# Kernel tuning notes

Measured on AMD Instinct MI355X. Metric: run time of the kernel, lower is better.

Reference implementation:

```python
import jax, jax.numpy as jnp
import numpy as np

HIDDEN = 2048
INTER = 1408
NUM_EXPERTS = 8
TOP_K = 2
BATCH, SEQ = 2, 1024


def setup_inputs() -> dict:
    key = jax.random.key(0)
    ks = jax.random.split(key, 8)
    s = 0.02
    return {
        "x": jax.random.normal(ks[0], (BATCH, SEQ, HIDDEN), dtype=jnp.float32),
        "router_w": jax.random.normal(ks[1], (NUM_EXPERTS, HIDDEN), dtype=jnp.float32) * s,
        "gate_w": jax.random.normal(ks[2], (NUM_EXPERTS, INTER, HIDDEN), dtype=jnp.float32) * s,
        "up_w": jax.random.normal(ks[3], (NUM_EXPERTS, INTER, HIDDEN), dtype=jnp.float32) * s,
        "down_w": jax.random.normal(ks[4], (NUM_EXPERTS, HIDDEN, INTER), dtype=jnp.float32) * s,
        "shared_gate_w": jax.random.normal(ks[5], (INTER, HIDDEN), dtype=jnp.float32) * s,
        "shared_up_w": jax.random.normal(ks[6], (INTER, HIDDEN), dtype=jnp.float32) * s,
        "shared_down_w": jax.random.normal(ks[7], (HIDDEN, INTER), dtype=jnp.float32) * s,
    }


def reference(x, router_w, gate_w, up_w, down_w,
              shared_gate_w, shared_up_w, shared_down_w):
    B, S, H = x.shape
    T = B * S
    E = router_w.shape[0]
    xf = x.reshape(T, H)

    # Router: softmax over experts, top-k selection, renormalized weights
    logits = xf @ router_w.T                       # [T, E]
    probs = jax.nn.softmax(logits, axis=-1)
    topw, topi = jax.lax.top_k(probs, TOP_K)       # [T, K]
    topw = topw / jnp.sum(topw, axis=-1, keepdims=True)

    # Combine weight per (token, expert): scatter-add of top-k weights
    comb = jnp.zeros((T, E), dtype=xf.dtype).at[
        jnp.arange(T)[:, None], topi].add(topw)    # [T, E]

    # All-expert SwiGLU (grouped GEMM form of masked gather/MLP/scatter)
    g = jnp.einsum('th,eih->tei', xf, gate_w)      # [T, E, I]
    u = jnp.einsum('th,eih->tei', xf, up_w)
    hmid = jax.nn.silu(g) * u
    eo = jnp.einsum('tei,ehi->teh', hmid, down_w)  # [T, E, H]
    out = jnp.einsum('te,teh->th', comb, eo)       # weighted combine

    # Shared expert applied to every token
    sh = (jax.nn.silu(xf @ shared_gate_w.T) * (xf @ shared_up_w.T)) @ shared_down_w.T
    out = out + sh
    return out.reshape(B, S, H)
```

## Files before the change

### kernel.cpp

```cpp
#include <hip/hip_runtime.h>
#include <cstdint>
#include <cstddef>

#define T_TOK 2048
#define HID   2048
#define INTER 1408
#define NEXP  8
#define NPAIR 6144
#define LDST  40

typedef __bf16 bf16x8 __attribute__((ext_vector_type(8)));
typedef float  floatx4 __attribute__((ext_vector_type(4)));

static const size_t XB_OFF   = 0;
static const size_t HM_OFF   = XB_OFF + (size_t)T_TOK * HID * 2;
static const size_t TOK_OFF  = HM_OFF + (size_t)NPAIR * INTER * 2;
static const size_t WGT_OFF  = TOK_OFF + (size_t)NPAIR * 4;
static const size_t TE_OFF   = WGT_OFF + (size_t)NPAIR * 4;
static const size_t TW_OFF   = TE_OFF + (size_t)T_TOK * 2 * 4;
static const size_t CTRL_OFF = TW_OFF + (size_t)T_TOK * 2 * 4;

static __device__ __forceinline__ unsigned short f2bf(float f) {
    unsigned u = __float_as_uint(f);
    u += 0x7fffu + ((u >> 16) & 1u);
    return (unsigned short)(u >> 16);
}
static __device__ __forceinline__ unsigned pk2(float a, float b) {
    return (unsigned)f2bf(a) | ((unsigned)f2bf(b) << 16);
}

__global__ __launch_bounds__(256) void k_cvt_x(const float* __restrict__ x,
                                               unsigned short* __restrict__ xb) {
    int gid = blockIdx.x * 256 + threadIdx.x;
    const float4* src = (const float4*)x;
    float4 a = src[gid * 2], b = src[gid * 2 + 1];
    uint4 o;
    o.x = pk2(a.x, a.y); o.y = pk2(a.z, a.w);
    o.z = pk2(b.x, b.y); o.w = pk2(b.z, b.w);
    ((uint4*)xb)[gid] = o;
}

__global__ __launch_bounds__(256) void k_router(const float* __restrict__ x,
                                                const float* __restrict__ rw,
                                                int* __restrict__ te, float* __restrict__ tw,
                                                int* __restrict__ counts) {
    int wave = threadIdx.x >> 6, lane = threadIdx.x & 63;
    int t = blockIdx.x * 4 + wave;
    const float* xp = x + (size_t)t * HID;

    float acc[8];
#pragma unroll
    for (int e = 0; e < 8; ++e) acc[e] = 0.f;
    for (int i = lane; i < HID; i += 64) {
        float xv = xp[i];
#pragma unroll
        for (int e = 0; e < 8; ++e) acc[e] = fmaf(xv, rw[e * HID + i], acc[e]);
    }
#pragma unroll
    for (int e = 0; e < 8; ++e) {
        float v = acc[e];
        for (int s = 32; s; s >>= 1) v += __shfl_xor(v, s, 64);
        acc[e] = v;
    }
    float mx = acc[0];
#pragma unroll
    for (int e = 1; e < 8; ++e) mx = fmaxf(mx, acc[e]);
    float p[8];
#pragma unroll
    for (int e = 0; e < 8; ++e) p[e] = __expf(acc[e] - mx);
    int i1 = 0; float v1 = p[0];
#pragma unroll
    for (int e = 1; e < 8; ++e) if (p[e] > v1) { v1 = p[e]; i1 = e; }
    int i2 = -1; float v2 = -1.f;
#pragma unroll
    for (int e = 0; e < 8; ++e) if (e != i1 && p[e] > v2) { v2 = p[e]; i2 = e; }
    float inv = 1.f / (v1 + v2);
    if (lane == 0) {
        te[2 * t] = i1;     tw[2 * t] = v1 * inv;
        te[2 * t + 1] = i2; tw[2 * t + 1] = v2 * inv;
        atomicAdd(&counts[i1], 1);
        atomicAdd(&counts[i2], 1);
    }
}

__global__ void k_offsets(int* __restrict__ ctrl) {
    if (threadIdx.x == 0) {
        int s = 0;
        for (int e = 0; e < 8; ++e) { ctrl[16 + e] = s; s += ctrl[e]; }
        ctrl[16 + 8] = s;
        ctrl[8] = T_TOK;
    }
}

__global__ __launch_bounds__(256) void k_scatter(const int* __restrict__ te,
                                                 const float* __restrict__ tw,
                                                 const int* __restrict__ offsets,
                                                 int* __restrict__ fill,
                                                 int* __restrict__ tok, float* __restrict__ wgt) {
    int t = blockIdx.x * 256 + threadIdx.x;
    if (t >= T_TOK) return;
#pragma unroll
    for (int k = 0; k < 2; ++k) {
        int e = te[2 * t + k];
        int slot = atomicAdd(&fill[e], 1);
        int pp = offsets[e] + slot;
        tok[pp] = t; wgt[pp] = tw[2 * t + k];
    }
    tok[2 * T_TOK + t] = t; wgt[2 * T_TOK + t] = 1.0f;
}

__global__ __launch_bounds__(256) void k_gemm1(const unsigned short* __restrict__ xb,
                                               const float* __restrict__ gate_w,
                                               const float* __restrict__ up_w,
                                               const float* __restrict__ sgate,
                                               const float* __restrict__ sup,
                                               const int* __restrict__ tok,
                                               const int* __restrict__ ctrl,
                                               unsigned short* __restrict__ hmid) {
    int e = blockIdx.z;
    int cnt = ctrl[e];
    int m0 = blockIdx.y * 128;
    if (m0 >= cnt) return;
    int off = ctrl[16 + e];
    int i0 = blockIdx.x * 64;
    const float* gw = (e < 8) ? gate_w + (size_t)e * INTER * HID : sgate;
    const float* uw = (e < 8) ? up_w + (size_t)e * INTER * HID : sup;

    __shared__ __align__(16) unsigned short As[128 * LDST];
    __shared__ __align__(16) unsigned short Bg[64 * LDST];
    __shared__ __align__(16) unsigned short Bu[64 * LDST];

    int tid = threadIdx.x;
    int lane = tid & 63, wave = tid >> 6;
    int ar = tid >> 1, ac = (tid & 1) * 16;
    int ap = off + m0 + ar; if (ap > NPAIR - 1) ap = NPAIR - 1;
    const unsigned short* asrc = xb + (size_t)tok[ap] * HID + ac;
    int br = tid >> 2, bc = (tid & 3) * 8;
    const float* gsrc = gw + (size_t)(i0 + br) * HID + bc;
    const float* usrc = uw + (size_t)(i0 + br) * HID + bc;

    floatx4 accg[2][4], accu[2][4];
#pragma unroll
    for (int mi = 0; mi < 2; ++mi)
#pragma unroll
        for (int ni = 0; ni < 4; ++ni) {
            accg[mi][ni] = (floatx4){0.f, 0.f, 0.f, 0.f};
            accu[mi][ni] = (floatx4){0.f, 0.f, 0.f, 0.f};
        }

    int wm = wave * 32;
    int mrow = lane & 15, kq = (lane >> 4) * 8;

    for (int kt = 0; kt < HID / 32; ++kt) {
        int h0 = kt * 32;
        uint4 av0 = *(const uint4*)(asrc + h0);
        uint4 av1 = *(const uint4*)(asrc + h0 + 8);
        float4 g0 = *(const float4*)(gsrc + h0);
        float4 g1 = *(const float4*)(gsrc + h0 + 4);
        float4 u0 = *(const float4*)(usrc + h0);
        float4 u1 = *(const float4*)(usrc + h0 + 4);
        __syncthreads();
        *(uint4*)&As[ar * LDST + ac] = av0;
        *(uint4*)&As[ar * LDST + ac + 8] = av1;
        uint4 bg; bg.x = pk2(g0.x, g0.y); bg.y = pk2(g0.z, g0.w);
        bg.z = pk2(g1.x, g1.y); bg.w = pk2(g1.z, g1.w);
        *(uint4*)&Bg[br * LDST + bc] = bg;
        uint4 bu; bu.x = pk2(u0.x, u0.y); bu.y = pk2(u0.z, u0.w);
        bu.z = pk2(u1.x, u1.y); bu.w = pk2(u1.z, u1.w);
        *(uint4*)&Bu[br * LDST + bc] = bu;
        __syncthreads();

        bf16x8 af[2];
#pragma unroll
        for (int mi = 0; mi < 2; ++mi)
            af[mi] = *(const bf16x8*)&As[(wm + mi * 16 + mrow) * LDST + kq];
#pragma unroll
        for (int ni = 0; ni < 4; ++ni) {
            bf16x8 bgv = *(const bf16x8*)&Bg[(ni * 16 + mrow) * LDST + kq];
            bf16x8 buv = *(const bf16x8*)&Bu[(ni * 16 + mrow) * LDST + kq];
#pragma unroll
            for (int mi = 0; mi < 2; ++mi) {
                accg[mi][ni] = __builtin_amdgcn_mfma_f32_16x16x32_bf16(af[mi], bgv, accg[mi][ni], 0, 0, 0);
                accu[mi][ni] = __builtin_amdgcn_mfma_f32_16x16x32_bf16(af[mi], buv, accu[mi][ni], 0, 0, 0);
            }
        }
    }

    int quad = lane >> 4, col = lane & 15;
#pragma unroll
    for (int mi = 0; mi < 2; ++mi)
#pragma unroll
        for (int ni = 0; ni < 4; ++ni)
#pragma unroll
            for (int r = 0; r < 4; ++r) {
                int row = m0 + wm + mi * 16 + quad * 4 + r;
                if (row < cnt) {
                    float g = accg[mi][ni][r], u = accu[mi][ni][r];
                    float s = g / (1.f + __expf(-g));
                    hmid[(size_t)(off + row) * INTER + i0 + ni * 16 + col] = f2bf(s * u);
                }
            }
}

__global__ __launch_bounds__(256) void k_gemm2(const unsigned short* __restrict__ hmid,
                                               const float* __restrict__ down_w,
                                               const float* __restrict__ sdown,
                                               const int* __restrict__ tok,
                                               const float* __restrict__ wgt,
                                               const int* __restrict__ ctrl,
                                               float* __restrict__ out) {
    int e = blockIdx.z;
    int cnt = ctrl[e];
    int m0 = blockIdx.y * 128;
    if (m0 >= cnt) return;
    int off = ctrl[16 + e];
    int n0 = blockIdx.x * 64;
    const float* dw = (e < 8) ? down_w + (size_t)e * HID * INTER : sdown;

    __shared__ __align__(16) unsigned short As[128 * LDST];
    __shared__ __align__(16) unsigned short Bd[64 * LDST];

    int tid = threadIdx.x;
    int lane = tid & 63, wave = tid >> 6;
    int ar = tid >> 1, ac = (tid & 1) * 16;
    int ap = off + m0 + ar; if (ap > NPAIR - 1) ap = NPAIR - 1;
    const unsigned short* asrc = hmid + (size_t)ap * INTER + ac;
    int br = tid >> 2, bc = (tid & 3) * 8;
    const float* bsrc = dw + (size_t)(n0 + br) * INTER + bc;

    floatx4 acc[2][4];
#pragma unroll
    for (int mi = 0; mi < 2; ++mi)
#pragma unroll
        for (int ni = 0; ni < 4; ++ni) acc[mi][ni] = (floatx4){0.f, 0.f, 0.f, 0.f};

    int wm = wave * 32;
    int mrow = lane & 15, kq = (lane >> 4) * 8;

    for (int kt = 0; kt < INTER / 32; ++kt) {
        int k0 = kt * 32;
        uint4 av0 = *(const uint4*)(asrc + k0);
        uint4 av1 = *(const uint4*)(asrc + k0 + 8);
        float4 b0 = *(const float4*)(bsrc + k0);
        float4 b1 = *(const float4*)(bsrc + k0 + 4);
        __syncthreads();
        *(uint4*)&As[ar * LDST + ac] = av0;
        *(uint4*)&As[ar * LDST + ac + 8] = av1;
        uint4 bd; bd.x = pk2(b0.x, b0.y); bd.y = pk2(b0.z, b0.w);
        bd.z = pk2(b1.x, b1.y); bd.w = pk2(b1.z, b1.w);
        *(uint4*)&Bd[br * LDST + bc] = bd;
        __syncthreads();

        bf16x8 af[2];
#pragma unroll
        for (int mi = 0; mi < 2; ++mi)
            af[mi] = *(const bf16x8*)&As[(wm + mi * 16 + mrow) * LDST + kq];
#pragma unroll
        for (int ni = 0; ni < 4; ++ni) {
            bf16x8 bv = *(const bf16x8*)&Bd[(ni * 16 + mrow) * LDST + kq];
#pragma unroll
            for (int mi = 0; mi < 2; ++mi)
                acc[mi][ni] = __builtin_amdgcn_mfma_f32_16x16x32_bf16(af[mi], bv, acc[mi][ni], 0, 0, 0);
        }
    }

    int quad = lane >> 4, col = lane & 15;
#pragma unroll
    for (int mi = 0; mi < 2; ++mi)
#pragma unroll
        for (int r = 0; r < 4; ++r) {
            int row = m0 + wm + mi * 16 + quad * 4 + r;
            if (row < cnt) {
                int p = off + row;
                int t = tok[p];
                float w = wgt[p];
#pragma unroll
                for (int ni = 0; ni < 4; ++ni)
                    atomicAdd(&out[(size_t)t * HID + n0 + ni * 16 + col], w * acc[mi][ni][r]);
            }
        }
}

extern "C" void kernel_launch(void* const* d_in, const int* in_sizes, int n_in,
                              void* d_out, int out_size, void* d_ws, size_t ws_size,
                              hipStream_t stream) {
    const float* x        = (const float*)d_in[0];
    const float* router_w = (const float*)d_in[1];
    const float* gate_w   = (const float*)d_in[2];
    const float* up_w     = (const float*)d_in[3];
    const float* down_w   = (const float*)d_in[4];
    const float* sgate    = (const float*)d_in[5];
    const float* sup      = (const float*)d_in[6];
    const float* sdown    = (const float*)d_in[7];
    float* out = (float*)d_out;

    char* ws = (char*)d_ws;
    unsigned short* xb   = (unsigned short*)(ws + XB_OFF);
    unsigned short* hmid = (unsigned short*)(ws + HM_OFF);
    int*   tok  = (int*)(ws + TOK_OFF);
    float* wgt  = (float*)(ws + WGT_OFF);
    int*   te   = (int*)(ws + TE_OFF);
    float* tw   = (float*)(ws + TW_OFF);
    int*   ctrl = (int*)(ws + CTRL_OFF);

    hipMemsetAsync(ctrl, 0, 48 * sizeof(int), stream);
    hipMemsetAsync(out, 0, (size_t)T_TOK * HID * sizeof(float), stream);

    k_cvt_x  <<<(T_TOK * HID) / 8 / 256, 256, 0, stream>>>(x, xb);
    k_router <<<T_TOK / 4, 256, 0, stream>>>(x, router_w, te, tw, ctrl);
    k_offsets<<<1, 64, 0, stream>>>(ctrl);
    k_scatter<<<T_TOK / 256, 256, 0, stream>>>(te, tw, ctrl + 16, ctrl + 32, tok, wgt);

    k_gemm1<<<dim3(INTER / 64, 16, 9), 256, 0, stream>>>(xb, gate_w, up_w, sgate, sup, tok, ctrl, hmid);
    k_gemm2<<<dim3(HID / 64, 16, 9), 256, 0, stream>>>(hmid, down_w, sdown, tok, wgt, ctrl, out);
}
```

Measured before the change: 629.6 us.

## Replace atomic scatter-add with bf16 per-pair outputs and a gather combine kernel

The down-projection GEMM now writes weighted per-pair results as bf16 into a workspace buffer instead of issuing float atomicAdds into the output, and a new combine kernel gathers each token's two expert rows plus the shared-expert row via an inverse index and sums them. This removes the output memset and the atomic contention. The GEMM grids are also reordered so that M tiles vary fastest, which changes weight-tile reuse across blocks, and the bf16 pack uses a hardware conversion builtin when one is available. In exchange it adds a large intermediate buffer write/read plus an extra launch, and rounds partial sums to bf16.

```diff
diff --git a/kernel.cpp b/kernel.cpp
--- a/kernel.cpp
+++ b/kernel.cpp
@@ -10,24 +10,34 @@
 #define LDST  40
 
 typedef __bf16 bf16x8 __attribute__((ext_vector_type(8)));
+typedef __bf16 bf16x2 __attribute__((ext_vector_type(2)));
 typedef float  floatx4 __attribute__((ext_vector_type(4)));
 
 static const size_t XB_OFF   = 0;
 static const size_t HM_OFF   = XB_OFF + (size_t)T_TOK * HID * 2;
-static const size_t TOK_OFF  = HM_OFF + (size_t)NPAIR * INTER * 2;
+static const size_t PO_OFF   = HM_OFF + (size_t)NPAIR * INTER * 2;
+static const size_t TOK_OFF  = PO_OFF + (size_t)NPAIR * HID * 2;
 static const size_t WGT_OFF  = TOK_OFF + (size_t)NPAIR * 4;
 static const size_t TE_OFF   = WGT_OFF + (size_t)NPAIR * 4;
 static const size_t TW_OFF   = TE_OFF + (size_t)T_TOK * 2 * 4;
-static const size_t CTRL_OFF = TW_OFF + (size_t)T_TOK * 2 * 4;
+static const size_t INV_OFF  = TW_OFF + (size_t)T_TOK * 2 * 4;
+static const size_t CTRL_OFF = INV_OFF + (size_t)T_TOK * 2 * 4;
 
 static __device__ __forceinline__ unsigned short f2bf(float f) {
     unsigned u = __float_as_uint(f);
     u += 0x7fffu + ((u >> 16) & 1u);
     return (unsigned short)(u >> 16);
 }
+#if __has_builtin(__builtin_amdgcn_cvt_pk_bf16_f32)
+static __device__ __forceinline__ unsigned pk2(float a, float b) {
+    bf16x2 v = __builtin_amdgcn_cvt_pk_bf16_f32(a, b);
+    return __builtin_bit_cast(unsigned, v);
+}
+#else
 static __device__ __forceinline__ unsigned pk2(float a, float b) {
     return (unsigned)f2bf(a) | ((unsigned)f2bf(b) << 16);
 }
+#endif
 
 __global__ __launch_bounds__(256) void k_cvt_x(const float* __restrict__ x,
                                                unsigned short* __restrict__ xb) {
@@ -96,7 +106,8 @@
                                                  const float* __restrict__ tw,
                                                  const int* __restrict__ offsets,
                                                  int* __restrict__ fill,
-                                                 int* __restrict__ tok, float* __restrict__ wgt) {
+                                                 int* __restrict__ tok, float* __restrict__ wgt,
+                                                 int* __restrict__ inv) {
     int t = blockIdx.x * 256 + threadIdx.x;
     if (t >= T_TOK) return;
 #pragma unroll
@@ -105,6 +116,7 @@
         int slot = atomicAdd(&fill[e], 1);
         int pp = offsets[e] + slot;
         tok[pp] = t; wgt[pp] = tw[2 * t + k];
+        inv[2 * t + k] = pp;
     }
     tok[2 * T_TOK + t] = t; wgt[2 * T_TOK + t] = 1.0f;
 }
@@ -119,10 +131,10 @@
                                                unsigned short* __restrict__ hmid) {
     int e = blockIdx.z;
     int cnt = ctrl[e];
-    int m0 = blockIdx.y * 128;
+    int m0 = blockIdx.x * 128;
     if (m0 >= cnt) return;
     int off = ctrl[16 + e];
-    int i0 = blockIdx.x * 64;
+    int i0 = blockIdx.y * 64;
     const float* gw = (e < 8) ? gate_w + (size_t)e * INTER * HID : sgate;
     const float* uw = (e < 8) ? up_w + (size_t)e * INTER * HID : sup;
 
@@ -205,16 +217,15 @@
 __global__ __launch_bounds__(256) void k_gemm2(const unsigned short* __restrict__ hmid,
                                                const float* __restrict__ down_w,
                                                const float* __restrict__ sdown,
-                                               const int* __restrict__ tok,
                                                const float* __restrict__ wgt,
                                                const int* __restrict__ ctrl,
-                                               float* __restrict__ out) {
+                                               unsigned short* __restrict__ pout) {
     int e = blockIdx.z;
     int cnt = ctrl[e];
-    int m0 = blockIdx.y * 128;
+    int m0 = blockIdx.x * 128;
     if (m0 >= cnt) return;
     int off = ctrl[16 + e];
-    int n0 = blockIdx.x * 64;
+    int n0 = blockIdx.y * 64;
     const float* dw = (e < 8) ? down_w + (size_t)e * HID * INTER : sdown;
 
     __shared__ __align__(16) unsigned short As[128 * LDST];
@@ -272,13 +283,36 @@
             int row = m0 + wm + mi * 16 + quad * 4 + r;
             if (row < cnt) {
                 int p = off + row;
-                int t = tok[p];
                 float w = wgt[p];
 #pragma unroll
                 for (int ni = 0; ni < 4; ++ni)
-                    atomicAdd(&out[(size_t)t * HID + n0 + ni * 16 + col], w * acc[mi][ni][r]);
+                    pout[(size_t)p * HID + n0 + ni * 16 + col] = f2bf(w * acc[mi][ni][r]);
             }
         }
+}
+
+__global__ __launch_bounds__(256) void k_combine(const unsigned short* __restrict__ pout,
+                                                 const int* __restrict__ inv,
+                                                 float* __restrict__ out) {
+    int gid = blockIdx.x * 256 + threadIdx.x;
+    int t = gid >> 8;
+    int h8 = (gid & 255) * 8;
+    int p0 = inv[2 * t], p1 = inv[2 * t + 1];
+    const uint4* pp = (const uint4*)pout;
+    uint4 a = pp[((size_t)p0 * HID + h8) >> 3];
+    uint4 b = pp[((size_t)p1 * HID + h8) >> 3];
+    uint4 c = pp[((size_t)(2 * T_TOK + t) * HID + h8) >> 3];
+    unsigned av[4] = {a.x, a.y, a.z, a.w}, bv[4] = {b.x, b.y, b.z, b.w}, cv[4] = {c.x, c.y, c.z, c.w};
+    float o[8];
+#pragma unroll
+    for (int i = 0; i < 4; ++i) {
+        o[2 * i]     = __uint_as_float(av[i] << 16) + __uint_as_float(bv[i] << 16) + __uint_as_float(cv[i] << 16);
+        o[2 * i + 1] = __uint_as_float(av[i] & 0xffff0000u) + __uint_as_float(bv[i] & 0xffff0000u)
+                     + __uint_as_float(cv[i] & 0xffff0000u);
+    }
+    float4* op = (float4*)(out + (size_t)t * HID + h8);
+    op[0] = (float4){o[0], o[1], o[2], o[3]};
+    op[1] = (float4){o[4], o[5], o[6], o[7]};
 }
 
 extern "C" void kernel_launch(void* const* d_in, const int* in_sizes, int n_in,
@@ -297,20 +331,22 @@
     char* ws = (char*)d_ws;
     unsigned short* xb   = (unsigned short*)(ws + XB_OFF);
     unsigned short* hmid = (unsigned short*)(ws + HM_OFF);
+    unsigned short* pout = (unsigned short*)(ws + PO_OFF);
     int*   tok  = (int*)(ws + TOK_OFF);
     float* wgt  = (float*)(ws + WGT_OFF);
     int*   te   = (int*)(ws + TE_OFF);
     float* tw   = (float*)(ws + TW_OFF);
+    int*   inv  = (int*)(ws + INV_OFF);
     int*   ctrl = (int*)(ws + CTRL_OFF);
 
-    hipMemsetAsync(ctrl, 0, 48 * sizeof(int), stream);
-    hipMemsetAsync(out, 0, (size_t)T_TOK * HID * sizeof(float), stream);
+    (void)hipMemsetAsync(ctrl, 0, 48 * sizeof(int), stream);
 
     k_cvt_x  <<<(T_TOK * HID) / 8 / 256, 256, 0, stream>>>(x, xb);
     k_router <<<T_TOK / 4, 256, 0, stream>>>(x, router_w, te, tw, ctrl);
     k_offsets<<<1, 64, 0, stream>>>(ctrl);
-    k_scatter<<<T_TOK / 256, 256, 0, stream>>>(te, tw, ctrl + 16, ctrl + 32, tok, wgt);
-
-    k_gemm1<<<dim3(INTER / 64, 16, 9), 256, 0, stream>>>(xb, gate_w, up_w, sgate, sup, tok, ctrl, hmid);
-    k_gemm2<<<dim3(HID / 64, 16, 9), 256, 0, stream>>>(hmid, down_w, sdown, tok, wgt, ctrl, out);
-}
+    k_scatter<<<T_TOK / 256, 256, 0, stream>>>(te, tw, ctrl + 16, ctrl + 32, tok, wgt, inv);
+
+    k_gemm1<<<dim3(16, INTER / 64, 9), 256, 0, stream>>>(xb, gate_w, up_w, sgate, sup, tok, ctrl, hmid);
+    k_gemm2<<<dim3(16, HID / 64, 9), 256, 0, stream>>>(hmid, down_w, sdown, wgt, ctrl, pout);
+    k_combine<<<(T_TOK * HID / 8) / 256, 256, 0, stream>>>(pout, inv, out);
+}
```

Result: slower. 974.4 us (+54.8%).
